# Kernel optimization log

Measured on AMD Instinct MI355X. Metric: run time of the kernel, lower is better.

The kernel has to match this reference:

```python
import jax, jax.numpy as jnp
import numpy as np

N_NODES = 50000
N_EDGES = 600000
D = 128        # input_dim == hidden_dim
OUT = 2        # output_dim
N_LAYERS = 6


def setup_inputs() -> dict:
    key = jax.random.key(0)
    ks = jax.random.split(key, 6)
    scale = 1.0 / np.sqrt(D)
    x = jax.random.normal(ks[0], (N_NODES, D), jnp.float32)
    edge_index = jax.random.randint(ks[1], (2, N_EDGES), 0, N_NODES)
    Wl = jax.random.normal(ks[2], (N_LAYERS, D, D), jnp.float32) * scale  # neighbor (lin_l) weights
    Wr = jax.random.normal(ks[3], (N_LAYERS, D, D), jnp.float32) * scale  # root (lin_r) weights
    bl = jnp.zeros((N_LAYERS, D), jnp.float32)                            # lin_l bias
    fc_W = jax.random.normal(ks[4], (D, OUT), jnp.float32) * scale
    fc_b = jnp.zeros((OUT,), jnp.float32)
    return {"x": x, "edge_index": edge_index, "Wl": Wl, "Wr": Wr, "bl": bl,
            "fc_W": fc_W, "fc_b": fc_b}


def _sage_conv(h, src, dst, deg_inv, Wl_i, Wr_i, bl_i):
    # mean aggregation over incoming edges: gather -> scatter-add -> normalize
    agg = jax.ops.segment_sum(h[src], dst, num_segments=h.shape[0]) * deg_inv  # [N, D]
    return agg @ Wl_i + h @ Wr_i + bl_i


def reference(x, edge_index, Wl, Wr, bl, fc_W, fc_b):
    src, dst = edge_index[0], edge_index[1]
    deg = jax.ops.segment_sum(jnp.ones(src.shape, x.dtype), dst, num_segments=x.shape[0])
    deg_inv = (1.0 / jnp.maximum(deg, 1.0))[:, None]  # [N, 1]
    h = x
    # ReLU follows every SAGEConv: inner act of each GraphSAGE block + explicit F.relu after each block
    for i in range(N_LAYERS):
        h = _sage_conv(h, src, dst, deg_inv, Wl[i], Wr[i], bl[i])
        h = jax.nn.relu(h)
    return h @ fc_W + fc_b  # [N, OUT]
```

## Files before the change

### kernel.cpp

```cpp
#include <hip/hip_runtime.h>
#include <hip/hip_bf16.h>

#define N_NODES 50000
#define N_EDGES 600000
#define DD 128
#define N_LAYERS 6
#define SCAN_BLOCKS 196
#define N_CHUNKS 3125
#define AGG_BLOCKS 6256

#define XB16_T 1600000
#define ZERO_T 50000
#define PREPW_T 196608
#define PREP_TOTAL (XB16_T + ZERO_T + PREPW_T)

typedef __attribute__((ext_vector_type(8))) short bf16x8;
typedef __attribute__((ext_vector_type(4))) float floatx4;

__device__ __forceinline__ unsigned short f2b(float f) {
    unsigned u = __float_as_uint(f);
    unsigned r = (u + 0x7FFFu + ((u >> 16) & 1u)) >> 16;
    return (unsigned short)r;
}


__global__ void prep_all(const float* __restrict__ x, unsigned short* __restrict__ hx,
                         const float* __restrict__ Wl, const float* __restrict__ Wr,
                         unsigned short* __restrict__ WT2,
                         int* __restrict__ deg, int* __restrict__ cursor) {
    int gid = blockIdx.x * blockDim.x + threadIdx.x;
    if (gid < XB16_T) {
        int b = gid * 4;
        float4 v = *(const float4*)(x + b);
        ushort4 o;
        o.x = f2b(v.x); o.y = f2b(v.y); o.z = f2b(v.z); o.w = f2b(v.w);
        *(ushort4*)(hx + b) = o;
    } else if (gid < XB16_T + ZERO_T) {
        int i = gid - XB16_T;
        deg[i] = 0; cursor[i] = 0;
    } else if (gid < PREP_TOTAL) {
        int idx = gid - (XB16_T + ZERO_T);
        int l   = idx >> 15;
        int rem = idx & 32767;
        int n   = rem >> 8;
        int k2  = rem & 255;
        const float* W = (k2 < 128 ? Wl : Wr) + (size_t)l * DD * DD + (size_t)(k2 & 127) * DD + n;
        WT2[idx] = f2b(*W);
    }
}


__global__ void count_deg(const int* __restrict__ dst, int* __restrict__ deg) {
    int e = blockIdx.x * blockDim.x + threadIdx.x;
    if (e < N_EDGES) atomicAdd(&deg[dst[e]], 1);
}

__global__ void block_sums(const int* __restrict__ deg, int* __restrict__ bsum) {
    __shared__ int s[256];
    int tid = threadIdx.x;
    int i = blockIdx.x * 256 + tid;
    int v = (i < N_NODES) ? deg[i] : 0;
    s[tid] = v;
    __syncthreads();
    #pragma unroll
    for (int off = 128; off > 0; off >>= 1) {
        if (tid < off) s[tid] += s[tid + off];
        __syncthreads();
    }
    if (tid == 0) bsum[blockIdx.x] = s[0];
}

__global__ void scan_bsums(int* __restrict__ bsum, int* __restrict__ offsets) {
    __shared__ int s[256];
    int tid = threadIdx.x;
    int v = (tid < SCAN_BLOCKS) ? bsum[tid] : 0;
    s[tid] = v;
    __syncthreads();
    for (int off = 1; off < 256; off <<= 1) {
        int t = (tid >= off) ? s[tid - off] : 0;
        __syncthreads();
        s[tid] += t;
        __syncthreads();
    }
    if (tid < SCAN_BLOCKS) bsum[tid] = s[tid] - v;
    if (tid == 0) offsets[N_NODES] = N_EDGES;
}

__global__ void write_offsets(const int* __restrict__ deg, const int* __restrict__ bsum,
                              int* __restrict__ offsets, float* __restrict__ deg_inv) {
    __shared__ int s[256];
    int tid = threadIdx.x;
    int i = blockIdx.x * 256 + tid;
    int v = (i < N_NODES) ? deg[i] : 0;
    s[tid] = v;
    __syncthreads();
    for (int off = 1; off < 256; off <<= 1) {
        int t = (tid >= off) ? s[tid - off] : 0;
        __syncthreads();
        s[tid] += t;
        __syncthreads();
    }
    if (i < N_NODES) {
        offsets[i] = bsum[blockIdx.x] + s[tid] - v;
        deg_inv[i] = 1.0f / (float)(v > 1 ? v : 1);
    }
}

__global__ void fill_csr(const int* __restrict__ src, const int* __restrict__ dst,
                         const int* __restrict__ offsets, int* __restrict__ cursor,
                         int* __restrict__ csr_src) {
    int e = blockIdx.x * blockDim.x + threadIdx.x;
    if (e < N_EDGES) {
        int d = dst[e];
        int p = atomicAdd(&cursor[d], 1);
        csr_src[offsets[d] + p] = src[e];
    }
}


__global__ void aggregate(const unsigned short* __restrict__ hin, const int* __restrict__ offsets,
                          const int* __restrict__ csr_src, const float* __restrict__ deg_inv,
                          unsigned short* __restrict__ agg) {
    int w    = threadIdx.x >> 6;
    int lane = threadIdx.x & 63;
    int nodeSel = lane >> 5;
    int l32  = lane & 31;
    int grp  = l32 >> 3;
    int p    = l32 & 7;

    int b = blockIdx.x;
    int x = b & 7, s = b >> 3;
    int hc = 16 * (s >> 1) + 2 * x + (s & 1);
    int node = hc * 8 + 2 * w + nodeSel;
    if (node >= N_NODES) return;
    int s0 = offsets[node], e0 = offsets[node + 1];
    float di = deg_inv[node];

    float a[16];
    #pragma unroll
    for (int i = 0; i < 16; ++i) a[i] = 0.f;

    const unsigned short* base = hin;
    int j = s0 + grp;
    for (; j + 4 < e0; j += 8) {
        int src1 = csr_src[j];
        int src2 = csr_src[j + 4];
        const uint4* r1 = (const uint4*)(base + (size_t)src1 * DD + p * 16);
        const uint4* r2 = (const uint4*)(base + (size_t)src2 * DD + p * 16);
        uint4 v1a = r1[0], v1b = r1[1];
        uint4 v2a = r2[0], v2b = r2[1];
        a[0] += __uint_as_float(v1a.x << 16); a[1] += __uint_as_float(v1a.x & 0xFFFF0000u);
        a[2] += __uint_as_float(v1a.y << 16); a[3] += __uint_as_float(v1a.y & 0xFFFF0000u);
        a[4] += __uint_as_float(v1a.z << 16); a[5] += __uint_as_float(v1a.z & 0xFFFF0000u);
        a[6] += __uint_as_float(v1a.w << 16); a[7] += __uint_as_float(v1a.w & 0xFFFF0000u);
        a[8] += __uint_as_float(v1b.x << 16); a[9] += __uint_as_float(v1b.x & 0xFFFF0000u);
        a[10]+= __uint_as_float(v1b.y << 16); a[11]+= __uint_as_float(v1b.y & 0xFFFF0000u);
        a[12]+= __uint_as_float(v1b.z << 16); a[13]+= __uint_as_float(v1b.z & 0xFFFF0000u);
        a[14]+= __uint_as_float(v1b.w << 16); a[15]+= __uint_as_float(v1b.w & 0xFFFF0000u);
        a[0] += __uint_as_float(v2a.x << 16); a[1] += __uint_as_float(v2a.x & 0xFFFF0000u);
        a[2] += __uint_as_float(v2a.y << 16); a[3] += __uint_as_float(v2a.y & 0xFFFF0000u);
        a[4] += __uint_as_float(v2a.z << 16); a[5] += __uint_as_float(v2a.z & 0xFFFF0000u);
        a[6] += __uint_as_float(v2a.w << 16); a[7] += __uint_as_float(v2a.w & 0xFFFF0000u);
        a[8] += __uint_as_float(v2b.x << 16); a[9] += __uint_as_float(v2b.x & 0xFFFF0000u);
        a[10]+= __uint_as_float(v2b.y << 16); a[11]+= __uint_as_float(v2b.y & 0xFFFF0000u);
        a[12]+= __uint_as_float(v2b.z << 16); a[13]+= __uint_as_float(v2b.z & 0xFFFF0000u);
        a[14]+= __uint_as_float(v2b.w << 16); a[15]+= __uint_as_float(v2b.w & 0xFFFF0000u);
    }
    if (j < e0) {
        int src1 = csr_src[j];
        const uint4* r1 = (const uint4*)(base + (size_t)src1 * DD + p * 16);
        uint4 v1a = r1[0], v1b = r1[1];
        a[0] += __uint_as_float(v1a.x << 16); a[1] += __uint_as_float(v1a.x & 0xFFFF0000u);
        a[2] += __uint_as_float(v1a.y << 16); a[3] += __uint_as_float(v1a.y & 0xFFFF0000u);
        a[4] += __uint_as_float(v1a.z << 16); a[5] += __uint_as_float(v1a.z & 0xFFFF0000u);
        a[6] += __uint_as_float(v1a.w << 16); a[7] += __uint_as_float(v1a.w & 0xFFFF0000u);
        a[8] += __uint_as_float(v1b.x << 16); a[9] += __uint_as_float(v1b.x & 0xFFFF0000u);
        a[10]+= __uint_as_float(v1b.y << 16); a[11]+= __uint_as_float(v1b.y & 0xFFFF0000u);
        a[12]+= __uint_as_float(v1b.z << 16); a[13]+= __uint_as_float(v1b.z & 0xFFFF0000u);
        a[14]+= __uint_as_float(v1b.w << 16); a[15]+= __uint_as_float(v1b.w & 0xFFFF0000u);
    }

    #pragma unroll
    for (int i = 0; i < 16; ++i) {
        a[i] += __shfl_xor(a[i], 8, 64);
        a[i] += __shfl_xor(a[i], 16, 64);
    }

    if (grp == 0) {
        uint4 o1, o2;
        o1.x = (unsigned)f2b(a[0] * di) | ((unsigned)f2b(a[1] * di) << 16);
        o1.y = (unsigned)f2b(a[2] * di) | ((unsigned)f2b(a[3] * di) << 16);
        o1.z = (unsigned)f2b(a[4] * di) | ((unsigned)f2b(a[5] * di) << 16);
        o1.w = (unsigned)f2b(a[6] * di) | ((unsigned)f2b(a[7] * di) << 16);
        o2.x = (unsigned)f2b(a[8] * di) | ((unsigned)f2b(a[9] * di) << 16);
        o2.y = (unsigned)f2b(a[10]* di) | ((unsigned)f2b(a[11]* di) << 16);
        o2.z = (unsigned)f2b(a[12]* di) | ((unsigned)f2b(a[13]* di) << 16);
        o2.w = (unsigned)f2b(a[14]* di) | ((unsigned)f2b(a[15]* di) << 16);
        uint4* dst = (uint4*)(agg + (size_t)node * DD + p * 16);
        dst[0] = o1;
        dst[1] = o2;
    }
}


__launch_bounds__(512, 4)
__global__ void gemm_resW(const unsigned short* __restrict__ Agg,
                          const unsigned short* __restrict__ H,
                          const unsigned short* __restrict__ WT2,
                          const float* __restrict__ bias,
                          unsigned short* __restrict__ Cout,
                          const float* __restrict__ fcW,
                          const float* __restrict__ fcb,
                          float* __restrict__ out,
                          int doFC) {
    __shared__ __align__(16) unsigned short sW[128 * 256];

    int tid  = threadIdx.x;
    int wid  = tid >> 6, lane = tid & 63;
    int l15  = lane & 15, q = lane >> 4;

    for (int t = tid; t < 4096; t += 512) {
        int col = t >> 5, c = t & 31;
        uint4 v = *(const uint4*)(WT2 + (size_t)col * 256 + c * 8);
        *(uint4*)(sW + ((size_t)col * 32 + (c ^ (col & 7))) * 8) = v;
    }
    __syncthreads();

    int chunk = blockIdx.x * 8 + wid;
    if (chunk >= N_CHUNKS) return;
    int row0 = chunk * 16;

    float bcol[8];
    #pragma unroll
    for (int j = 0; j < 8; ++j) bcol[j] = bias[j * 16 + l15];

    const unsigned short* Arow = Agg + (size_t)(row0 + l15) * DD;
    const unsigned short* Hrow = H   + (size_t)(row0 + l15) * DD;
    bf16x8 aF[8];
    #pragma unroll
    for (int s = 0; s < 4; ++s)
        aF[s] = *(const bf16x8*)(Arow + (s * 4 + q) * 8);
    #pragma unroll
    for (int s = 4; s < 8; ++s)
        aF[s] = *(const bf16x8*)(Hrow + (s * 4 + q - 16) * 8);

    floatx4 acc[8];
    #pragma unroll
    for (int j = 0; j < 8; ++j) acc[j] = (floatx4){0.f, 0.f, 0.f, 0.f};

    #pragma unroll
    for (int s = 0; s < 8; ++s) {
        int cglob = s * 4 + q;
        #pragma unroll
        for (int j = 0; j < 8; ++j) {
            int col = j * 16 + l15;
            bf16x8 bF = *(const bf16x8*)(sW + ((size_t)col * 32 + (cglob ^ (col & 7))) * 8);
            acc[j] = __builtin_amdgcn_mfma_f32_16x16x32_bf16(aF[s], bF, acc[j], 0, 0, 0);
        }
    }

    if (!doFC) {
        #pragma unroll
        for (int r = 0; r < 4; ++r) {
            int row = row0 + q * 4 + r;
            #pragma unroll
            for (int j = 0; j < 8; ++j) {
                float v = acc[j][r] + bcol[j];
                Cout[(size_t)row * DD + j * 16 + l15] = f2b(fmaxf(v, 0.f));
            }
        }
    } else {
        float2 fcw[8];
        #pragma unroll
        for (int j = 0; j < 8; ++j) fcw[j] = *(const float2*)(fcW + (j * 16 + l15) * 2);
        float fb0 = fcb[0], fb1 = fcb[1];
        #pragma unroll
        for (int r = 0; r < 4; ++r) {
            float p0 = 0.f, p1 = 0.f;
            #pragma unroll
            for (int j = 0; j < 8; ++j) {
                float v = fmaxf(acc[j][r] + bcol[j], 0.f);
                p0 += v * fcw[j].x;
                p1 += v * fcw[j].y;
            }
            p0 += __shfl_xor(p0, 1, 64); p1 += __shfl_xor(p1, 1, 64);
            p0 += __shfl_xor(p0, 2, 64); p1 += __shfl_xor(p1, 2, 64);
            p0 += __shfl_xor(p0, 4, 64); p1 += __shfl_xor(p1, 4, 64);
            p0 += __shfl_xor(p0, 8, 64); p1 += __shfl_xor(p1, 8, 64);
            if (l15 == 0) {
                int row = row0 + q * 4 + r;
                out[row * 2]     = p0 + fb0;
                out[row * 2 + 1] = p1 + fb1;
            }
        }
    }
}


extern "C" void kernel_launch(void* const* d_in, const int* in_sizes, int n_in,
                              void* d_out, int out_size, void* d_ws, size_t ws_size,
                              hipStream_t stream) {
    const float* x    = (const float*)d_in[0];
    const int*   ei   = (const int*)d_in[1];
    const float* Wl   = (const float*)d_in[2];
    const float* Wr   = (const float*)d_in[3];
    const float* bl   = (const float*)d_in[4];
    const float* fcW  = (const float*)d_in[5];
    const float* fcb  = (const float*)d_in[6];
    float* out = (float*)d_out;

    const int* srcIdx = ei;
    const int* dstIdx = ei + N_EDGES;

    char* ws = (char*)d_ws;
    size_t off = 0;
    auto bump = [&](size_t bytes) { char* p = ws + off; off = (off + bytes + 255) & ~(size_t)255; return p; };
    int*   deg     = (int*)  bump(N_NODES * 4);
    int*   cursor  = (int*)  bump(N_NODES * 4);
    int*   offsets = (int*)  bump((N_NODES + 1) * 4);
    int*   bsum    = (int*)  bump(SCAN_BLOCKS * 4);
    float* deg_inv = (float*)bump(N_NODES * 4);
    int*   csr     = (int*)  bump(N_EDGES * 4);
    unsigned short* hx   = (unsigned short*)bump((size_t)N_NODES * DD * 2);
    unsigned short* hb0  = (unsigned short*)bump((size_t)N_NODES * DD * 2);
    unsigned short* hb1  = (unsigned short*)bump((size_t)N_NODES * DD * 2);
    unsigned short* agg  = (unsigned short*)bump((size_t)N_NODES * DD * 2);
    unsigned short* WT2  = (unsigned short*)bump((size_t)N_LAYERS * 128 * 256 * 2);
    (void)ws_size;

    prep_all<<<(PREP_TOTAL + 255) / 256, 256, 0, stream>>>(x, hx, Wl, Wr, WT2, deg, cursor);
    count_deg<<<(N_EDGES + 255) / 256, 256, 0, stream>>>(dstIdx, deg);
    block_sums<<<SCAN_BLOCKS, 256, 0, stream>>>(deg, bsum);
    scan_bsums<<<1, 256, 0, stream>>>(bsum, offsets);
    write_offsets<<<SCAN_BLOCKS, 256, 0, stream>>>(deg, bsum, offsets, deg_inv);
    fill_csr<<<(N_EDGES + 255) / 256, 256, 0, stream>>>(srcIdx, dstIdx, offsets, cursor, csr);

    const unsigned short* hin = hx;
    unsigned short* hbuf[2] = { hb0, hb1 };
    for (int l = 0; l < N_LAYERS; ++l) {
        int last = (l == N_LAYERS - 1);
        aggregate<<<AGG_BLOCKS, 256, 0, stream>>>(hin, offsets, csr, deg_inv, agg);
        unsigned short* hout = hbuf[l & 1];
        gemm_resW<<<(N_CHUNKS + 7) / 8, 512, 0, stream>>>(
            agg, hin, WT2 + (size_t)l * 128 * 256, bl + (size_t)l * DD, hout,
            fcW, fcb, out, last);
        hin = hout;
    }
}
```

Before: 341.8 us.

## Fuse neighbor aggregation into per-layer GEMM kernel

Merges the separate aggregate kernel into the GEMM kernel so each wave first gathers and mean-aggregates its own 16 rows, writes them to the agg buffer, then runs the MFMA GEMM over those rows. This removes one kernel launch per layer and lets the aggregated rows be re-read while still warm in cache. In exchange, the gather now runs under the GEMM's launch bounds and occupancy, with only about 391 blocks, and each wave processes 8 node pairs serially, so latency hiding for the irregular gathers may drop. It also relies on a waitcnt to make the wave's own global writes visible to its later reads.

```diff
diff --git a/kernel.cpp b/kernel.cpp
--- a/kernel.cpp
+++ b/kernel.cpp
@@ -7,7 +7,6 @@
 #define N_LAYERS 6
 #define SCAN_BLOCKS 196
 #define N_CHUNKS 3125
-#define AGG_BLOCKS 6256
 
 #define XB16_T 1600000
 #define ZERO_T 50000
@@ -118,106 +117,23 @@
 }
 
 
-__global__ void aggregate(const unsigned short* __restrict__ hin, const int* __restrict__ offsets,
-                          const int* __restrict__ csr_src, const float* __restrict__ deg_inv,
-                          unsigned short* __restrict__ agg) {
-    int w    = threadIdx.x >> 6;
-    int lane = threadIdx.x & 63;
-    int nodeSel = lane >> 5;
-    int l32  = lane & 31;
-    int grp  = l32 >> 3;
-    int p    = l32 & 7;
-
-    int b = blockIdx.x;
-    int x = b & 7, s = b >> 3;
-    int hc = 16 * (s >> 1) + 2 * x + (s & 1);
-    int node = hc * 8 + 2 * w + nodeSel;
-    if (node >= N_NODES) return;
-    int s0 = offsets[node], e0 = offsets[node + 1];
-    float di = deg_inv[node];
-
-    float a[16];
-    #pragma unroll
-    for (int i = 0; i < 16; ++i) a[i] = 0.f;
-
-    const unsigned short* base = hin;
-    int j = s0 + grp;
-    for (; j + 4 < e0; j += 8) {
-        int src1 = csr_src[j];
-        int src2 = csr_src[j + 4];
-        const uint4* r1 = (const uint4*)(base + (size_t)src1 * DD + p * 16);
-        const uint4* r2 = (const uint4*)(base + (size_t)src2 * DD + p * 16);
-        uint4 v1a = r1[0], v1b = r1[1];
-        uint4 v2a = r2[0], v2b = r2[1];
-        a[0] += __uint_as_float(v1a.x << 16); a[1] += __uint_as_float(v1a.x & 0xFFFF0000u);
-        a[2] += __uint_as_float(v1a.y << 16); a[3] += __uint_as_float(v1a.y & 0xFFFF0000u);
-        a[4] += __uint_as_float(v1a.z << 16); a[5] += __uint_as_float(v1a.z & 0xFFFF0000u);
-        a[6] += __uint_as_float(v1a.w << 16); a[7] += __uint_as_float(v1a.w & 0xFFFF0000u);
-        a[8] += __uint_as_float(v1b.x << 16); a[9] += __uint_as_float(v1b.x & 0xFFFF0000u);
-        a[10]+= __uint_as_float(v1b.y << 16); a[11]+= __uint_as_float(v1b.y & 0xFFFF0000u);
-        a[12]+= __uint_as_float(v1b.z << 16); a[13]+= __uint_as_float(v1b.z & 0xFFFF0000u);
-        a[14]+= __uint_as_float(v1b.w << 16); a[15]+= __uint_as_float(v1b.w & 0xFFFF0000u);
-        a[0] += __uint_as_float(v2a.x << 16); a[1] += __uint_as_float(v2a.x & 0xFFFF0000u);
-        a[2] += __uint_as_float(v2a.y << 16); a[3] += __uint_as_float(v2a.y & 0xFFFF0000u);
-        a[4] += __uint_as_float(v2a.z << 16); a[5] += __uint_as_float(v2a.z & 0xFFFF0000u);
-        a[6] += __uint_as_float(v2a.w << 16); a[7] += __uint_as_float(v2a.w & 0xFFFF0000u);
-        a[8] += __uint_as_float(v2b.x << 16); a[9] += __uint_as_float(v2b.x & 0xFFFF0000u);
-        a[10]+= __uint_as_float(v2b.y << 16); a[11]+= __uint_as_float(v2b.y & 0xFFFF0000u);
-        a[12]+= __uint_as_float(v2b.z << 16); a[13]+= __uint_as_float(v2b.z & 0xFFFF0000u);
-        a[14]+= __uint_as_float(v2b.w << 16); a[15]+= __uint_as_float(v2b.w & 0xFFFF0000u);
-    }
-    if (j < e0) {
-        int src1 = csr_src[j];
-        const uint4* r1 = (const uint4*)(base + (size_t)src1 * DD + p * 16);
-        uint4 v1a = r1[0], v1b = r1[1];
-        a[0] += __uint_as_float(v1a.x << 16); a[1] += __uint_as_float(v1a.x & 0xFFFF0000u);
-        a[2] += __uint_as_float(v1a.y << 16); a[3] += __uint_as_float(v1a.y & 0xFFFF0000u);
-        a[4] += __uint_as_float(v1a.z << 16); a[5] += __uint_as_float(v1a.z & 0xFFFF0000u);
-        a[6] += __uint_as_float(v1a.w << 16); a[7] += __uint_as_float(v1a.w & 0xFFFF0000u);
-        a[8] += __uint_as_float(v1b.x << 16); a[9] += __uint_as_float(v1b.x & 0xFFFF0000u);
-        a[10]+= __uint_as_float(v1b.y << 16); a[11]+= __uint_as_float(v1b.y & 0xFFFF0000u);
-        a[12]+= __uint_as_float(v1b.z << 16); a[13]+= __uint_as_float(v1b.z & 0xFFFF0000u);
-        a[14]+= __uint_as_float(v1b.w << 16); a[15]+= __uint_as_float(v1b.w & 0xFFFF0000u);
-    }
-
-    #pragma unroll
-    for (int i = 0; i < 16; ++i) {
-        a[i] += __shfl_xor(a[i], 8, 64);
-        a[i] += __shfl_xor(a[i], 16, 64);
-    }
-
-    if (grp == 0) {
-        uint4 o1, o2;
-        o1.x = (unsigned)f2b(a[0] * di) | ((unsigned)f2b(a[1] * di) << 16);
-        o1.y = (unsigned)f2b(a[2] * di) | ((unsigned)f2b(a[3] * di) << 16);
-        o1.z = (unsigned)f2b(a[4] * di) | ((unsigned)f2b(a[5] * di) << 16);
-        o1.w = (unsigned)f2b(a[6] * di) | ((unsigned)f2b(a[7] * di) << 16);
-        o2.x = (unsigned)f2b(a[8] * di) | ((unsigned)f2b(a[9] * di) << 16);
-        o2.y = (unsigned)f2b(a[10]* di) | ((unsigned)f2b(a[11]* di) << 16);
-        o2.z = (unsigned)f2b(a[12]* di) | ((unsigned)f2b(a[13]* di) << 16);
-        o2.w = (unsigned)f2b(a[14]* di) | ((unsigned)f2b(a[15]* di) << 16);
-        uint4* dst = (uint4*)(agg + (size_t)node * DD + p * 16);
-        dst[0] = o1;
-        dst[1] = o2;
-    }
-}
-
-
 __launch_bounds__(512, 4)
-__global__ void gemm_resW(const unsigned short* __restrict__ Agg,
-                          const unsigned short* __restrict__ H,
-                          const unsigned short* __restrict__ WT2,
-                          const float* __restrict__ bias,
-                          unsigned short* __restrict__ Cout,
-                          const float* __restrict__ fcW,
-                          const float* __restrict__ fcb,
-                          float* __restrict__ out,
-                          int doFC) {
+__global__ void sage_layer(const unsigned short* __restrict__ H,
+                           const int* __restrict__ offsets,
+                           const int* __restrict__ csr_src,
+                           const float* __restrict__ deg_inv,
+                           const unsigned short* __restrict__ WT2,
+                           const float* __restrict__ bias,
+                           unsigned short* __restrict__ agg,
+                           unsigned short* __restrict__ Cout,
+                           const float* __restrict__ fcW,
+                           const float* __restrict__ fcb,
+                           float* __restrict__ out,
+                           int doFC) {
     __shared__ __align__(16) unsigned short sW[128 * 256];
 
     int tid  = threadIdx.x;
     int wid  = tid >> 6, lane = tid & 63;
-    int l15  = lane & 15, q = lane >> 4;
 
     for (int t = tid; t < 4096; t += 512) {
         int col = t >> 5, c = t & 31;
@@ -230,11 +146,91 @@
     if (chunk >= N_CHUNKS) return;
     int row0 = chunk * 16;
 
+    {
+        int nodeSel = lane >> 5;
+        int l32  = lane & 31;
+        int grp  = l32 >> 3;
+        int p    = l32 & 7;
+
+        for (int it = 0; it < 8; ++it) {
+            int node = row0 + it * 2 + nodeSel;
+            int s0 = offsets[node], e0 = offsets[node + 1];
+            float di = deg_inv[node];
+
+            float a[16];
+            #pragma unroll
+            for (int i = 0; i < 16; ++i) a[i] = 0.f;
+
+            int j = s0 + grp;
+            for (; j + 4 < e0; j += 8) {
+                int src1 = csr_src[j];
+                int src2 = csr_src[j + 4];
+                const uint4* r1 = (const uint4*)(H + (size_t)src1 * DD + p * 16);
+                const uint4* r2 = (const uint4*)(H + (size_t)src2 * DD + p * 16);
+                uint4 v1a = r1[0], v1b = r1[1];
+                uint4 v2a = r2[0], v2b = r2[1];
+                a[0] += __uint_as_float(v1a.x << 16); a[1] += __uint_as_float(v1a.x & 0xFFFF0000u);
+                a[2] += __uint_as_float(v1a.y << 16); a[3] += __uint_as_float(v1a.y & 0xFFFF0000u);
+                a[4] += __uint_as_float(v1a.z << 16); a[5] += __uint_as_float(v1a.z & 0xFFFF0000u);
+                a[6] += __uint_as_float(v1a.w << 16); a[7] += __uint_as_float(v1a.w & 0xFFFF0000u);
+                a[8] += __uint_as_float(v1b.x << 16); a[9] += __uint_as_float(v1b.x & 0xFFFF0000u);
+                a[10]+= __uint_as_float(v1b.y << 16); a[11]+= __uint_as_float(v1b.y & 0xFFFF0000u);
+                a[12]+= __uint_as_float(v1b.z << 16); a[13]+= __uint_as_float(v1b.z & 0xFFFF0000u);
+                a[14]+= __uint_as_float(v1b.w << 16); a[15]+= __uint_as_float(v1b.w & 0xFFFF0000u);
+                a[0] += __uint_as_float(v2a.x << 16); a[1] += __uint_as_float(v2a.x & 0xFFFF0000u);
+                a[2] += __uint_as_float(v2a.y << 16); a[3] += __uint_as_float(v2a.y & 0xFFFF0000u);
+                a[4] += __uint_as_float(v2a.z << 16); a[5] += __uint_as_float(v2a.z & 0xFFFF0000u);
+                a[6] += __uint_as_float(v2a.w << 16); a[7] += __uint_as_float(v2a.w & 0xFFFF0000u);
+                a[8] += __uint_as_float(v2b.x << 16); a[9] += __uint_as_float(v2b.x & 0xFFFF0000u);
+                a[10]+= __uint_as_float(v2b.y << 16); a[11]+= __uint_as_float(v2b.y & 0xFFFF0000u);
+                a[12]+= __uint_as_float(v2b.z << 16); a[13]+= __uint_as_float(v2b.z & 0xFFFF0000u);
+                a[14]+= __uint_as_float(v2b.w << 16); a[15]+= __uint_as_float(v2b.w & 0xFFFF0000u);
+            }
+            if (j < e0) {
+                int src1 = csr_src[j];
+                const uint4* r1 = (const uint4*)(H + (size_t)src1 * DD + p * 16);
+                uint4 v1a = r1[0], v1b = r1[1];
+                a[0] += __uint_as_float(v1a.x << 16); a[1] += __uint_as_float(v1a.x & 0xFFFF0000u);
+                a[2] += __uint_as_float(v1a.y << 16); a[3] += __uint_as_float(v1a.y & 0xFFFF0000u);
+                a[4] += __uint_as_float(v1a.z << 16); a[5] += __uint_as_float(v1a.z & 0xFFFF0000u);
+                a[6] += __uint_as_float(v1a.w << 16); a[7] += __uint_as_float(v1a.w & 0xFFFF0000u);
+                a[8] += __uint_as_float(v1b.x << 16); a[9] += __uint_as_float(v1b.x & 0xFFFF0000u);
+                a[10]+= __uint_as_float(v1b.y << 16); a[11]+= __uint_as_float(v1b.y & 0xFFFF0000u);
+                a[12]+= __uint_as_float(v1b.z << 16); a[13]+= __uint_as_float(v1b.z & 0xFFFF0000u);
+                a[14]+= __uint_as_float(v1b.w << 16); a[15]+= __uint_as_float(v1b.w & 0xFFFF0000u);
+            }
+
+            #pragma unroll
+            for (int i = 0; i < 16; ++i) {
+                a[i] += __shfl_xor(a[i], 8, 64);
+                a[i] += __shfl_xor(a[i], 16, 64);
+            }
+
+            if (grp == 0) {
+                uint4 o1, o2;
+                o1.x = (unsigned)f2b(a[0] * di) | ((unsigned)f2b(a[1] * di) << 16);
+                o1.y = (unsigned)f2b(a[2] * di) | ((unsigned)f2b(a[3] * di) << 16);
+                o1.z = (unsigned)f2b(a[4] * di) | ((unsigned)f2b(a[5] * di) << 16);
+                o1.w = (unsigned)f2b(a[6] * di) | ((unsigned)f2b(a[7] * di) << 16);
+                o2.x = (unsigned)f2b(a[8] * di) | ((unsigned)f2b(a[9] * di) << 16);
+                o2.y = (unsigned)f2b(a[10]* di) | ((unsigned)f2b(a[11]* di) << 16);
+                o2.z = (unsigned)f2b(a[12]* di) | ((unsigned)f2b(a[13]* di) << 16);
+                o2.w = (unsigned)f2b(a[14]* di) | ((unsigned)f2b(a[15]* di) << 16);
+                uint4* dst = (uint4*)(agg + (size_t)node * DD + p * 16);
+                dst[0] = o1;
+                dst[1] = o2;
+            }
+        }
+    }
+    __builtin_amdgcn_s_waitcnt(0);
+
+    int l15 = lane & 15, q = lane >> 4;
+
     float bcol[8];
     #pragma unroll
     for (int j = 0; j < 8; ++j) bcol[j] = bias[j * 16 + l15];
 
-    const unsigned short* Arow = Agg + (size_t)(row0 + l15) * DD;
+    const unsigned short* Arow = agg + (size_t)(row0 + l15) * DD;
     const unsigned short* Hrow = H   + (size_t)(row0 + l15) * DD;
     bf16x8 aF[8];
     #pragma unroll
@@ -339,11 +335,10 @@
     unsigned short* hbuf[2] = { hb0, hb1 };
     for (int l = 0; l < N_LAYERS; ++l) {
         int last = (l == N_LAYERS - 1);
-        aggregate<<<AGG_BLOCKS, 256, 0, stream>>>(hin, offsets, csr, deg_inv, agg);
         unsigned short* hout = hbuf[l & 1];
-        gemm_resW<<<(N_CHUNKS + 7) / 8, 512, 0, stream>>>(
-            agg, hin, WT2 + (size_t)l * 128 * 256, bl + (size_t)l * DD, hout,
-            fcW, fcb, out, last);
+        sage_layer<<<(N_CHUNKS + 7) / 8, 512, 0, stream>>>(
+            hin, offsets, csr, deg_inv, WT2 + (size_t)l * 128 * 256, bl + (size_t)l * DD,
+            agg, hout, fcW, fcb, out, last);
         hin = hout;
     }
 }
```

Measured after the change: 370.0 us. 8.2% more time.
